# Optimization experiments

Hardware: AMD Instinct MI355X
Metric: run time of the kernel (lower is better)

Reference implementation:

```python
import jax, jax.numpy as jnp
import numpy as np

B, T, C = 4, 2048, 1024
H = 16
D = C // H  # head_dim = 64


def setup_inputs() -> dict:
    key = jax.random.key(0)
    ks = jax.random.split(key, 11)
    s = 0.02
    return {
        "q": jax.random.normal(ks[0], (B, T, C), jnp.float32),
        "k": jax.random.normal(ks[1], (B, T, C), jnp.float32),
        "v": jax.random.normal(ks[2], (B, T, C), jnp.float32),
        "Wq": jax.random.normal(ks[3], (C, C), jnp.float32) * s,
        "bq": jnp.zeros((C,), jnp.float32),
        "Wk": jax.random.normal(ks[4], (C, C), jnp.float32) * s,
        "bk": jnp.zeros((C,), jnp.float32),
        "Wv": jax.random.normal(ks[5], (C, C), jnp.float32) * s,
        "bv": jnp.zeros((C,), jnp.float32),
        "Wo": jax.random.normal(ks[6], (C, C), jnp.float32) * s,
        "bo": jnp.zeros((C,), jnp.float32),
    }


def reference(q, k, v, Wq, bq, Wk, bk, Wv, bv, Wo, bo):
    # projections (torch Linear: x @ W.T + b)
    qh = (q @ Wq.T + bq).reshape(B, T, H, D).transpose(0, 2, 1, 3)  # [B,H,T,D]
    kh = (k @ Wk.T + bk).reshape(B, T, H, D).transpose(0, 2, 1, 3)
    vh = (v @ Wv.T + bv).reshape(B, T, H, D).transpose(0, 2, 1, 3)
    scores = jnp.einsum('bhqd,bhkd->bhqk', qh, kh) * (D ** -0.5)  # [B,H,T,T]
    # causal mask (is_causal=True)
    causal = jnp.tril(jnp.ones((T, T), bool))
    scores = jnp.where(causal, scores, -jnp.inf)
    probs = jax.nn.softmax(scores, axis=-1)
    # dropout_rate=0.0 -> identity in eval mode
    out = jnp.einsum('bhqk,bhkd->bhqd', probs, vh)  # [B,H,T,D]
    out = out.transpose(0, 2, 1, 3).reshape(B, T, C)
    return out @ Wo.T + bo
```

## Files before the change

kernel.cpp:

```cpp
#include <hip/hip_runtime.h>
#include <hip/hip_bf16.h>

typedef __attribute__((ext_vector_type(8))) short bf16x8;
typedef __attribute__((ext_vector_type(4))) float f32x4;
typedef __attribute__((ext_vector_type(16))) float f32x16;

__device__ __forceinline__ unsigned short f2bf(float x) {
  union { float f; unsigned u; } v; v.f = x;
  unsigned r = v.u + 0x7fffu + ((v.u >> 16) & 1u);
  return (unsigned short)(r >> 16);
}

__device__ __forceinline__ unsigned cvtpk_bf16(float lo, float hi) {
  unsigned r;
  asm("v_cvt_pk_bf16_f32 %0, %1, %2" : "=v"(r) : "v"(lo), "v"(hi));
  return r;
}
__device__ __forceinline__ void pl32swap(unsigned &a, unsigned &b) {
  asm volatile("v_permlane32_swap_b32 %0, %1" : "+v"(a), "+v"(b));
}

__device__ __forceinline__ void gload_lds16(const void* g, void* l) {
  __builtin_amdgcn_global_load_lds((const __attribute__((address_space(1))) void*)g,
                                   (__attribute__((address_space(3))) void*)l, 16, 0, 0);
}

#define SWZ(x) ((x) ^ ((((x) >> 7) & 7) << 4))

__global__ __launch_bounds__(256) void cvt_w(
    const float* __restrict__ W0, const float* __restrict__ W1,
    const float* __restrict__ W2, const float* __restrict__ W3,
    unsigned short* __restrict__ o0, unsigned short* __restrict__ o1,
    unsigned short* __restrict__ o2, unsigned short* __restrict__ o3,
    float s0) {
  const int z = blockIdx.y;
  const float* W = (z == 0) ? W0 : (z == 1) ? W1 : (z == 2) ? W2 : W3;
  unsigned short* o = (z == 0) ? o0 : (z == 1) ? o1 : (z == 2) ? o2 : o3;
  const float s = (z == 0) ? s0 : 1.0f;
  const int i = blockIdx.x * 256 + threadIdx.x;
  const float4 x = ((const float4*)W)[i];
  uint2 u;
  u.x = cvtpk_bf16(x.x * s, x.y * s);
  u.y = cvtpk_bf16(x.z * s, x.w * s);
  ((uint2*)o)[i] = u;
}


__global__ __launch_bounds__(256) void proj_gemm3(
    const float* __restrict__ A0, const float* __restrict__ A1, const float* __restrict__ A2,
    const unsigned short* __restrict__ W0b, const unsigned short* __restrict__ W1b,
    const unsigned short* __restrict__ W2b,
    const float* __restrict__ b0, const float* __restrict__ b1, const float* __restrict__ b2,
    unsigned short* __restrict__ o0, unsigned short* __restrict__ o1,
    unsigned short* __restrict__ o2) {
  const int K = 1024;
  __shared__ __align__(16) unsigned short As[2][4096];
  __shared__ __align__(16) unsigned short Bs[2][4096];
  const int z = blockIdx.z;
  const float* A = (z == 0) ? A0 : (z == 1) ? A1 : A2;
  const unsigned short* Wb = (z == 0) ? W0b : (z == 1) ? W1b : W2b;
  const float* bias = (z == 0) ? b0 : (z == 1) ? b1 : b2;
  unsigned short* out = (z == 0) ? o0 : (z == 1) ? o1 : o2;
  const float bscale = (z == 0) ? 0.125f * 1.4426950408889634f : 1.0f;
  const int vtrans = (z == 2);

  const int tid = threadIdx.x;
  const int row0 = blockIdx.x * 128;
  const int col0 = blockIdx.y * 128;
  const int lane = tid & 63;
  const int w = tid >> 6;
  const int wm = (w >> 1) * 64, wn = (w & 1) * 64;
  const int fr = lane & 15;
  const int g = lane >> 4;
  const int frh = fr >> 1;
  const int gcf = ((fr & 1) * 4 + g) ^ frh;
  const int aoff = wm * 64 + frh * 128 + gcf * 16;
  const int boff = wn * 64 + frh * 128 + gcf * 16;

  const int ar = tid >> 2;
  const int acq = tid & 3;
  const float* asrc0 = &A[(size_t)(row0 + ar) * K + acq * 8];
  const float* asrc1 = asrc0 + (size_t)64 * K;
  const int awr = (ar >> 1) * 128 + ((((ar & 1) * 4 + acq) ^ ((ar >> 1) & 7)) * 16);

  const unsigned short* bsrc[2];
  int bldso[2];
#pragma unroll
  for (int j = 0; j < 2; ++j) {
    const int L = (w * 2 + j) * 64 + lane;
    const int pp = L >> 3, gc = L & 7;
    const int e = gc ^ (pp & 7);
    const int r = pp * 2 + (e >> 2), c = e & 3;
    bsrc[j] = Wb + (size_t)(col0 + r) * K + c * 8;
    bldso[j] = (w * 2 + j) * 1024;
  }

  f32x4 acc[4][4] = {};
  float4 la[4];

  auto loadA = [&](int kt) {
    const float* s0 = asrc0 + kt * 32;
    const float* s1 = asrc1 + kt * 32;
    la[0] = *(const float4*)s0; la[1] = *(const float4*)(s0 + 4);
    la[2] = *(const float4*)s1; la[3] = *(const float4*)(s1 + 4);
  };
  auto storeA = [&](int buf) {
    uint4 u0, u1;
    u0.x = cvtpk_bf16(la[0].x, la[0].y); u0.y = cvtpk_bf16(la[0].z, la[0].w);
    u0.z = cvtpk_bf16(la[1].x, la[1].y); u0.w = cvtpk_bf16(la[1].z, la[1].w);
    u1.x = cvtpk_bf16(la[2].x, la[2].y); u1.y = cvtpk_bf16(la[2].z, la[2].w);
    u1.z = cvtpk_bf16(la[3].x, la[3].y); u1.w = cvtpk_bf16(la[3].z, la[3].w);
    char* base = (char*)As[buf];
    *(uint4*)(base + awr) = u0;
    *(uint4*)(base + awr + 4096) = u1;
  };
  auto stageB = [&](int buf, int kt) {
#pragma unroll
    for (int j = 0; j < 2; ++j)
      gload_lds16(bsrc[j] + kt * 32, (char*)Bs[buf] + bldso[j]);
  };

  loadA(0); stageB(0, 0); storeA(0);
  __syncthreads();
  for (int kt = 0; kt < 32; ++kt) {
    const int buf = kt & 1;
    if (kt < 31) { loadA(kt + 1); stageB(buf ^ 1, kt + 1); }
    const char* Ab = (const char*)As[buf];
    const char* Bb = (const char*)Bs[buf];
    bf16x8 af[4], bfv[4];
#pragma unroll
    for (int i = 0; i < 4; ++i) {
      af[i] = *(const bf16x8*)(Ab + aoff + i * 1024);
      bfv[i] = *(const bf16x8*)(Bb + boff + i * 1024);
    }
#pragma unroll
    for (int i = 0; i < 4; ++i)
#pragma unroll
      for (int j = 0; j < 4; ++j)
        acc[i][j] = __builtin_amdgcn_mfma_f32_16x16x32_bf16(af[i], bfv[j], acc[i][j], 0, 0, 0);
    if (kt < 31) storeA(buf ^ 1);
    __syncthreads();
  }

#pragma unroll
  for (int j = 0; j < 4; ++j) {
    const int n = col0 + wn + j * 16 + fr;
    const float bv = bias[n] * bscale;
    const int h = n >> 6, d = n & 63;
#pragma unroll
    for (int i = 0; i < 4; ++i) {
      const int mrow = row0 + wm + i * 16 + g * 4;
      const int b = mrow >> 11, t0 = mrow & 2047;
      if (vtrans) {
        uint2 u;
        u.x = cvtpk_bf16(acc[i][j][0] + bv, acc[i][j][1] + bv);
        u.y = cvtpk_bf16(acc[i][j][2] + bv, acc[i][j][3] + bv);
        *(uint2*)(&out[(((size_t)b * 16 + h) * 64 + d) * 2048 + t0]) = u;
      } else {
#pragma unroll
        for (int r = 0; r < 4; ++r)
          out[(((size_t)b * 16 + h) * 2048 + (t0 + r)) * 64 + d] = f2bf(acc[i][j][r] + bv);
      }
    }
  }
}

__global__ __launch_bounds__(256) void out_gemm(
    const unsigned short* __restrict__ A, const unsigned short* __restrict__ Wb,
    const float* __restrict__ bias, float* __restrict__ out) {
  const int K = 1024;
  __shared__ __align__(16) unsigned short As[2][4096];
  __shared__ __align__(16) unsigned short Bs[2][4096];
  const int tid = threadIdx.x;
  const int row0 = blockIdx.x * 128;
  const int col0 = blockIdx.y * 128;
  const int lane = tid & 63;
  const int w = tid >> 6;
  const int wm = (w >> 1) * 64, wn = (w & 1) * 64;
  const int fr = lane & 15;
  const int g = lane >> 4;
  const int frh = fr >> 1;
  const int gcf = ((fr & 1) * 4 + g) ^ frh;
  const int aoff = wm * 64 + frh * 128 + gcf * 16;
  const int boff = wn * 64 + frh * 128 + gcf * 16;

  const unsigned short* asrc[2];
  const unsigned short* bsrc[2];
  int ldso[2];
#pragma unroll
  for (int j = 0; j < 2; ++j) {
    const int L = (w * 2 + j) * 64 + lane;
    const int pp = L >> 3, gc = L & 7;
    const int e = gc ^ (pp & 7);
    const int r = pp * 2 + (e >> 2), c = e & 3;
    asrc[j] = A + (size_t)(row0 + r) * K + c * 8;
    bsrc[j] = Wb + (size_t)(col0 + r) * K + c * 8;
    ldso[j] = (w * 2 + j) * 1024;
  }

  f32x4 acc[4][4] = {};

  auto stage = [&](int buf, int kt) {
#pragma unroll
    for (int j = 0; j < 2; ++j) {
      gload_lds16(asrc[j] + kt * 32, (char*)As[buf] + ldso[j]);
      gload_lds16(bsrc[j] + kt * 32, (char*)Bs[buf] + ldso[j]);
    }
  };

  stage(0, 0);
  __syncthreads();
  for (int kt = 0; kt < 32; ++kt) {
    const int buf = kt & 1;
    if (kt < 31) stage(buf ^ 1, kt + 1);
    const char* Ab = (const char*)As[buf];
    const char* Bb = (const char*)Bs[buf];
    bf16x8 af[4], bfv[4];
#pragma unroll
    for (int i = 0; i < 4; ++i) {
      af[i] = *(const bf16x8*)(Ab + aoff + i * 1024);
      bfv[i] = *(const bf16x8*)(Bb + boff + i * 1024);
    }
#pragma unroll
    for (int i = 0; i < 4; ++i)
#pragma unroll
      for (int j = 0; j < 4; ++j)
        acc[i][j] = __builtin_amdgcn_mfma_f32_16x16x32_bf16(af[i], bfv[j], acc[i][j], 0, 0, 0);
    __syncthreads();
  }

#pragma unroll
  for (int j = 0; j < 4; ++j) {
    const int n = col0 + wn + j * 16 + fr;
    const float bv = bias[n];
#pragma unroll
    for (int i = 0; i < 4; ++i) {
      const int mrow = row0 + wm + i * 16 + g * 4;
#pragma unroll
      for (int r = 0; r < 4; ++r)
        out[(size_t)(mrow + r) * 1024 + n] = acc[i][j][r] + bv;
    }
  }
}

__global__ __launch_bounds__(256) void attn_mfma(
    const unsigned short* __restrict__ qh, const unsigned short* __restrict__ kh,
    const unsigned short* __restrict__ vT, unsigned short* __restrict__ Ob) {
  __shared__ __align__(16) unsigned short Klds[2][64 * 64];
  __shared__ __align__(16) unsigned short Vlds[2][64 * 64];

  const int tid = threadIdx.x;
  const int lane = tid & 63;
  const int w = tid >> 6;
  const int bh = blockIdx.y;
  const int b = bh >> 4, h = bh & 15;
  const int q32 = lane & 31;
  const int hi = lane >> 5;

  const char* kbase = (const char*)(kh + (size_t)bh * 2048 * 64);
  const char* vbase = (const char*)(vT + (size_t)bh * 64 * 2048);

  const int lrow = lane >> 3;
  const int cb = (((lane & 7) ^ lrow) << 4);

  auto stage = [&](int buf, int t) {
    const int kv0 = t * 64;
#pragma unroll
    for (int j = 0; j < 2; ++j) {
      const int c = w * 2 + j;
      const int r = c * 8 + lrow;
      gload_lds16(kbase + (size_t)(kv0 + r) * 128 + cb,
                  (char*)Klds[buf] + c * 1024);
      gload_lds16(vbase + (size_t)r * 4096 + (size_t)kv0 * 2 + cb,
                  (char*)Vlds[buf] + c * 1024);
    }
  };

  for (int pass = 0; pass < 2; ++pass) {
    const int qt = pass == 0 ? (15 - (int)blockIdx.x) : (int)blockIdx.x;
    const int qb = qt * 128 + w * 32;
    const int nt = 2 * qt + 2;

    bf16x8 qf[4];
    {
      const unsigned short* qp = qh + ((size_t)bh * 2048 + qb + q32) * 64;
#pragma unroll
      for (int kk = 0; kk < 4; ++kk)
        qf[kk] = *(const bf16x8*)(qp + kk * 16 + hi * 8);
    }

    f32x16 acc_o[2] = {};
    float m_run = -INFINITY, l_run = 0.f;

    stage(0, 0);
    __syncthreads();

    int cur = 0;
    for (int t = 0; t < nt; ++t) {
      const int kv0 = t * 64;
      if (t + 1 < nt) stage(cur ^ 1, t + 1);

      if (kv0 < qb + 32) {
        const char* Kb = (const char*)Klds[cur];
        const char* Vb = (const char*)Vlds[cur];

        f32x16 sacc[2] = {};
        __builtin_amdgcn_s_setprio(1);
#pragma unroll
        for (int kk = 0; kk < 4; ++kk) {
          bf16x8 kf0 = *(const bf16x8*)(Kb + SWZ((q32) * 128 + kk * 32 + hi * 16));
          bf16x8 kf1 = *(const bf16x8*)(Kb + SWZ((32 + q32) * 128 + kk * 32 + hi * 16));
          sacc[0] = __builtin_amdgcn_mfma_f32_32x32x16_bf16(kf0, qf[kk], sacc[0], 0, 0, 0);
          sacc[1] = __builtin_amdgcn_mfma_f32_32x32x16_bf16(kf1, qf[kk], sacc[1], 0, 0, 0);
        }
        __builtin_amdgcn_s_setprio(0);

        if (kv0 + 64 > qb) {
          const int qa = qb + q32;
#pragma unroll
          for (int mkv = 0; mkv < 2; ++mkv)
#pragma unroll
            for (int r = 0; r < 16; ++r) {
              const int kva = kv0 + mkv * 32 + 4 * hi + (r & 3) + 8 * (r >> 2);
              if (kva > qa) sacc[mkv][r] = -INFINITY;
            }
        }

        float mx = -INFINITY;
#pragma unroll
        for (int mkv = 0; mkv < 2; ++mkv)
#pragma unroll
          for (int r = 0; r < 16; ++r) mx = fmaxf(mx, sacc[mkv][r]);
        mx = fmaxf(mx, __shfl_xor(mx, 32));
        if (!__all(mx <= m_run + 8.f)) {
          const float mnew = fmaxf(m_run, mx);
          const float al = exp2f(m_run - mnew);
          m_run = mnew;
          l_run *= al;
          acc_o[0] = acc_o[0] * al;
          acc_o[1] = acc_o[1] * al;
        }

        float ls = 0.f;
        unsigned W[2][8];
#pragma unroll
        for (int mkv = 0; mkv < 2; ++mkv)
#pragma unroll
          for (int s = 0; s < 8; ++s) {
            const float p0 = exp2f(sacc[mkv][2 * s] - m_run);
            const float p1 = exp2f(sacc[mkv][2 * s + 1] - m_run);
            ls += p0 + p1;
            W[mkv][s] = cvtpk_bf16(p0, p1);
          }
        ls += __shfl_xor(ls, 32);
        l_run += ls;

#pragma unroll
        for (int mkv = 0; mkv < 2; ++mkv) {
          pl32swap(W[mkv][0], W[mkv][2]);
          pl32swap(W[mkv][1], W[mkv][3]);
          pl32swap(W[mkv][4], W[mkv][6]);
          pl32swap(W[mkv][5], W[mkv][7]);
        }

        __builtin_amdgcn_s_setprio(1);
#pragma unroll
        for (int wg = 0; wg < 4; ++wg) {
          union { unsigned u[4]; bf16x8 v; } pk;
          pk.u[0] = W[wg >> 1][(wg & 1) * 4 + 0];
          pk.u[1] = W[wg >> 1][(wg & 1) * 4 + 1];
          pk.u[2] = W[wg >> 1][(wg & 1) * 4 + 2];
          pk.u[3] = W[wg >> 1][(wg & 1) * 4 + 3];
          bf16x8 vf0 = *(const bf16x8*)(Vb + SWZ((q32) * 128 + wg * 32 + hi * 16));
          bf16x8 vf1 = *(const bf16x8*)(Vb + SWZ((32 + q32) * 128 + wg * 32 + hi * 16));
          acc_o[0] = __builtin_amdgcn_mfma_f32_32x32x16_bf16(vf0, pk.v, acc_o[0], 0, 0, 0);
          acc_o[1] = __builtin_amdgcn_mfma_f32_32x32x16_bf16(vf1, pk.v, acc_o[1], 0, 0, 0);
        }
        __builtin_amdgcn_s_setprio(0);
      }

      __syncthreads();
      cur ^= 1;
    }

    {
      const float inv = 1.0f / l_run;
      const int qa = qb + q32;
      unsigned short* op = Ob + ((size_t)b * 2048 + qa) * 1024 + h * 64;
#pragma unroll
      for (int md = 0; md < 2; ++md)
#pragma unroll
        for (int rr = 0; rr < 4; ++rr) {
          uint2 u;
          u.x = cvtpk_bf16(acc_o[md][rr * 4 + 0] * inv, acc_o[md][rr * 4 + 1] * inv);
          u.y = cvtpk_bf16(acc_o[md][rr * 4 + 2] * inv, acc_o[md][rr * 4 + 3] * inv);
          *(uint2*)(op + md * 32 + rr * 8 + hi * 4) = u;
        }
    }
  }
}

extern "C" void kernel_launch(void* const* d_in, const int* in_sizes, int n_in,
                              void* d_out, int out_size, void* d_ws, size_t ws_size,
                              hipStream_t stream) {
  (void)in_sizes; (void)n_in; (void)out_size; (void)ws_size;
  const float* q = (const float*)d_in[0];
  const float* k = (const float*)d_in[1];
  const float* v = (const float*)d_in[2];
  const float* Wq = (const float*)d_in[3];
  const float* bq = (const float*)d_in[4];
  const float* Wk = (const float*)d_in[5];
  const float* bk = (const float*)d_in[6];
  const float* Wv = (const float*)d_in[7];
  const float* bv = (const float*)d_in[8];
  const float* Wo = (const float*)d_in[9];
  const float* bo = (const float*)d_in[10];
  float* out = (float*)d_out;

  const size_t SZ = (size_t)4 * 16 * 2048 * 64;
  const size_t WSZ = (size_t)1024 * 1024;
  unsigned short* qh = (unsigned short*)d_ws;
  unsigned short* kh = qh + SZ;
  unsigned short* vT = kh + SZ;
  unsigned short* Ob = vT + SZ;
  unsigned short* Wqb = Ob + SZ;
  unsigned short* Wkb = Wqb + WSZ;
  unsigned short* Wvb = Wkb + WSZ;
  unsigned short* Wob = Wvb + WSZ;

  dim3 g0(1024, 4), b0(256);
  cvt_w<<<g0, b0, 0, stream>>>(Wq, Wk, Wv, Wo, Wqb, Wkb, Wvb, Wob,
                               0.125f * 1.4426950408889634f);

  dim3 g1(64, 8, 3), b1(256);
  proj_gemm3<<<g1, b1, 0, stream>>>(q, k, v, Wqb, Wkb, Wvb, bq, bk, bv, qh, kh, vT);

  dim3 g2(8, 64), b2(256);
  attn_mfma<<<g2, b2, 0, stream>>>(qh, kh, vT, Ob);

  dim3 g3(64, 8), b3(256);
  out_gemm<<<g3, b3, 0, stream>>>(Ob, Wob, bo, out);
}
```

Measured before the change: 223.7 us.

## Triple-buffer LDS in projection and output GEMMs with explicit vmcnt waits

Both projection and output GEMMs move from double to triple LDS buffering. Each now prefetches two k-tiles ahead and uses manual s_waitcnt vmcnt plus raw s_barrier instead of __syncthreads. The projection GEMM ping-pongs two register sets for the fp32 A loads so conversion and storing lag one tile behind the loads. This aims to hide global load latency behind MFMA work, at the cost of more LDS per block, which may lower occupancy, and fragile hand-counted wait values.

```diff
diff --git a/kernel.cpp b/kernel.cpp
--- a/kernel.cpp
+++ b/kernel.cpp
@@ -19,7 +19,6 @@
 __device__ __forceinline__ void pl32swap(unsigned &a, unsigned &b) {
   asm volatile("v_permlane32_swap_b32 %0, %1" : "+v"(a), "+v"(b));
 }
-
 __device__ __forceinline__ void gload_lds16(const void* g, void* l) {
   __builtin_amdgcn_global_load_lds((const __attribute__((address_space(1))) void*)g,
                                    (__attribute__((address_space(3))) void*)l, 16, 0, 0);
@@ -54,8 +53,9 @@
     unsigned short* __restrict__ o0, unsigned short* __restrict__ o1,
     unsigned short* __restrict__ o2) {
   const int K = 1024;
-  __shared__ __align__(16) unsigned short As[2][4096];
-  __shared__ __align__(16) unsigned short Bs[2][4096];
+  const int NK = 32;
+  __shared__ __align__(16) unsigned short As[3][4096];
+  __shared__ __align__(16) unsigned short Bs[3][4096];
   const int z = blockIdx.z;
   const float* A = (z == 0) ? A0 : (z == 1) ? A1 : A2;
   const unsigned short* Wb = (z == 0) ? W0b : (z == 1) ? W1b : W2b;
@@ -96,51 +96,92 @@
   }
 
   f32x4 acc[4][4] = {};
-  float4 la[4];
-
-  auto loadA = [&](int kt) {
-    const float* s0 = asrc0 + kt * 32;
-    const float* s1 = asrc1 + kt * 32;
-    la[0] = *(const float4*)s0; la[1] = *(const float4*)(s0 + 4);
-    la[2] = *(const float4*)s1; la[3] = *(const float4*)(s1 + 4);
-  };
-  auto storeA = [&](int buf) {
-    uint4 u0, u1;
-    u0.x = cvtpk_bf16(la[0].x, la[0].y); u0.y = cvtpk_bf16(la[0].z, la[0].w);
-    u0.z = cvtpk_bf16(la[1].x, la[1].y); u0.w = cvtpk_bf16(la[1].z, la[1].w);
-    u1.x = cvtpk_bf16(la[2].x, la[2].y); u1.y = cvtpk_bf16(la[2].z, la[2].w);
-    u1.z = cvtpk_bf16(la[3].x, la[3].y); u1.w = cvtpk_bf16(la[3].z, la[3].w);
-    char* base = (char*)As[buf];
-    *(uint4*)(base + awr) = u0;
-    *(uint4*)(base + awr + 4096) = u1;
-  };
-  auto stageB = [&](int buf, int kt) {
-#pragma unroll
-    for (int j = 0; j < 2; ++j)
-      gload_lds16(bsrc[j] + kt * 32, (char*)Bs[buf] + bldso[j]);
-  };
-
-  loadA(0); stageB(0, 0); storeA(0);
-  __syncthreads();
-  for (int kt = 0; kt < 32; ++kt) {
-    const int buf = kt & 1;
-    if (kt < 31) { loadA(kt + 1); stageB(buf ^ 1, kt + 1); }
-    const char* Ab = (const char*)As[buf];
-    const char* Bb = (const char*)Bs[buf];
-    bf16x8 af[4], bfv[4];
-#pragma unroll
-    for (int i = 0; i < 4; ++i) {
-      af[i] = *(const bf16x8*)(Ab + aoff + i * 1024);
-      bfv[i] = *(const bf16x8*)(Bb + boff + i * 1024);
-    }
-#pragma unroll
-    for (int i = 0; i < 4; ++i)
-#pragma unroll
-      for (int j = 0; j < 4; ++j)
-        acc[i][j] = __builtin_amdgcn_mfma_f32_16x16x32_bf16(af[i], bfv[j], acc[i][j], 0, 0, 0);
-    if (kt < 31) storeA(buf ^ 1);
-    __syncthreads();
-  }
+  float4 la0[4], la1[4];
+
+#define LOADA(kt, LA)                                        \
+  {                                                          \
+    const float* s0_ = asrc0 + (kt) * 32;                    \
+    const float* s1_ = asrc1 + (kt) * 32;                    \
+    LA[0] = *(const float4*)s0_; LA[1] = *(const float4*)(s0_ + 4); \
+    LA[2] = *(const float4*)s1_; LA[3] = *(const float4*)(s1_ + 4); \
+  }
+#define STOREA(buf, LA)                                               \
+  {                                                                   \
+    uint4 u0_, u1_;                                                   \
+    u0_.x = cvtpk_bf16(LA[0].x, LA[0].y); u0_.y = cvtpk_bf16(LA[0].z, LA[0].w); \
+    u0_.z = cvtpk_bf16(LA[1].x, LA[1].y); u0_.w = cvtpk_bf16(LA[1].z, LA[1].w); \
+    u1_.x = cvtpk_bf16(LA[2].x, LA[2].y); u1_.y = cvtpk_bf16(LA[2].z, LA[2].w); \
+    u1_.z = cvtpk_bf16(LA[3].x, LA[3].y); u1_.w = cvtpk_bf16(LA[3].z, LA[3].w); \
+    char* base_ = (char*)As[buf];                                     \
+    *(uint4*)(base_ + awr) = u0_;                                     \
+    *(uint4*)(base_ + awr + 4096) = u1_;                              \
+  }
+#define STAGEB(buf, kt)                                               \
+  {                                                                   \
+    gload_lds16(bsrc[0] + (kt) * 32, (char*)Bs[buf] + bldso[0]);      \
+    gload_lds16(bsrc[1] + (kt) * 32, (char*)Bs[buf] + bldso[1]);      \
+  }
+#define COMPUTE(cb)                                                   \
+  {                                                                   \
+    const char* Ab_ = (const char*)As[cb];                            \
+    const char* Bb_ = (const char*)Bs[cb];                            \
+    bf16x8 af[4], bfv[4];                                             \
+    _Pragma("unroll")                                                 \
+    for (int i = 0; i < 4; ++i) {                                     \
+      af[i] = *(const bf16x8*)(Ab_ + aoff + i * 1024);                \
+      bfv[i] = *(const bf16x8*)(Bb_ + boff + i * 1024);               \
+    }                                                                 \
+    _Pragma("unroll")                                                 \
+    for (int i = 0; i < 4; ++i)                                       \
+      _Pragma("unroll")                                               \
+      for (int j = 0; j < 4; ++j)                                     \
+        acc[i][j] = __builtin_amdgcn_mfma_f32_16x16x32_bf16(af[i], bfv[j], acc[i][j], 0, 0, 0); \
+  }
+
+  STAGEB(0, 0); STAGEB(1, 1);
+  LOADA(0, la0); LOADA(1, la1);
+  STOREA(0, la0);
+  asm volatile("s_waitcnt lgkmcnt(0)" ::: "memory");
+
+  int cur = 0;
+  for (int kt = 0; kt < NK; kt += 2) {
+    if (kt == 0) asm volatile("s_waitcnt vmcnt(0)" ::: "memory");
+    else         asm volatile("s_waitcnt vmcnt(6)" ::: "memory");
+    __builtin_amdgcn_sched_barrier(0);
+    __builtin_amdgcn_s_barrier();
+    __builtin_amdgcn_sched_barrier(0);
+    {
+      const int nx1 = (cur == 2) ? 0 : cur + 1;
+      const int nx2 = (nx1 == 2) ? 0 : nx1 + 1;
+      if (kt + 2 < NK) { LOADA(kt + 2, la0); STAGEB(nx2, kt + 2); }
+      __builtin_amdgcn_sched_barrier(0);
+      COMPUTE(cur);
+      STOREA(nx1, la1);
+      asm volatile("s_waitcnt lgkmcnt(0)" ::: "memory");
+      cur = nx1;
+    }
+    if (kt + 1 == NK - 1) asm volatile("s_waitcnt vmcnt(0)" ::: "memory");
+    else                  asm volatile("s_waitcnt vmcnt(6)" ::: "memory");
+    __builtin_amdgcn_sched_barrier(0);
+    __builtin_amdgcn_s_barrier();
+    __builtin_amdgcn_sched_barrier(0);
+    {
+      const int nx1 = (cur == 2) ? 0 : cur + 1;
+      const int nx2 = (nx1 == 2) ? 0 : nx1 + 1;
+      if (kt + 3 < NK) { LOADA(kt + 3, la1); STAGEB(nx2, kt + 3); }
+      __builtin_amdgcn_sched_barrier(0);
+      COMPUTE(cur);
+      if (kt + 2 < NK) {
+        STOREA(nx1, la0);
+        asm volatile("s_waitcnt lgkmcnt(0)" ::: "memory");
+      }
+      cur = nx1;
+    }
+  }
+#undef LOADA
+#undef STOREA
+#undef STAGEB
+#undef COMPUTE
 
 #pragma unroll
   for (int j = 0; j < 4; ++j) {
@@ -169,8 +210,9 @@
     const unsigned short* __restrict__ A, const unsigned short* __restrict__ Wb,
     const float* __restrict__ bias, float* __restrict__ out) {
   const int K = 1024;
-  __shared__ __align__(16) unsigned short As[2][4096];
-  __shared__ __align__(16) unsigned short Bs[2][4096];
+  const int NK = 32;
+  __shared__ __align__(16) unsigned short As[3][4096];
+  __shared__ __align__(16) unsigned short Bs[3][4096];
   const int tid = threadIdx.x;
   const int row0 = blockIdx.x * 128;
   const int col0 = blockIdx.y * 128;
@@ -208,13 +250,20 @@
     }
   };
 
-  stage(0, 0);
-  __syncthreads();
-  for (int kt = 0; kt < 32; ++kt) {
-    const int buf = kt & 1;
-    if (kt < 31) stage(buf ^ 1, kt + 1);
-    const char* Ab = (const char*)As[buf];
-    const char* Bb = (const char*)Bs[buf];
+  stage(0, 0); stage(1, 1);
+  int cur = 0;
+  for (int kt = 0; kt < NK; ++kt) {
+    if (kt == 0 || kt == NK - 1) asm volatile("s_waitcnt vmcnt(0)" ::: "memory");
+    else                         asm volatile("s_waitcnt vmcnt(4)" ::: "memory");
+    __builtin_amdgcn_sched_barrier(0);
+    __builtin_amdgcn_s_barrier();
+    __builtin_amdgcn_sched_barrier(0);
+    const int nx1 = (cur == 2) ? 0 : cur + 1;
+    const int nx2 = (nx1 == 2) ? 0 : nx1 + 1;
+    if (kt + 2 < NK) stage(nx2, kt + 2);
+    __builtin_amdgcn_sched_barrier(0);
+    const char* Ab = (const char*)As[cur];
+    const char* Bb = (const char*)Bs[cur];
     bf16x8 af[4], bfv[4];
 #pragma unroll
     for (int i = 0; i < 4; ++i) {
@@ -226,7 +275,7 @@
 #pragma unroll
       for (int j = 0; j < 4; ++j)
         acc[i][j] = __builtin_amdgcn_mfma_f32_16x16x32_bf16(af[i], bfv[j], acc[i][j], 0, 0, 0);
-    __syncthreads();
+    cur = nx1;
   }
 
 #pragma unroll
```

Result: faster. 201.2 us (-10.1%).

## Pre-convert activations to bf16 and use direct-to-LDS loads with BK=64 tiles

Applied to the files above, without the earlier changes.

Adds a separate kernel that converts the q/k/v fp32 activations to bf16 in workspace. The projection GEMM can then stage A through global_load_lds like B, instead of loading fp32 into registers, converting, and storing to LDS. Both GEMMs double the K-tile to 64, halving the number of barriers, and raise wave priority around the MFMA blocks. The cost is an extra launch plus a full fp32 read and bf16 write/read of the activations, and twice the LDS per block.

```diff
diff --git a/kernel.cpp b/kernel.cpp
--- a/kernel.cpp
+++ b/kernel.cpp
@@ -19,7 +19,6 @@
 __device__ __forceinline__ void pl32swap(unsigned &a, unsigned &b) {
   asm volatile("v_permlane32_swap_b32 %0, %1" : "+v"(a), "+v"(b));
 }
-
 __device__ __forceinline__ void gload_lds16(const void* g, void* l) {
   __builtin_amdgcn_global_load_lds((const __attribute__((address_space(1))) void*)g,
                                    (__attribute__((address_space(3))) void*)l, 16, 0, 0);
@@ -45,19 +44,37 @@
   ((uint2*)o)[i] = u;
 }
 
+__global__ __launch_bounds__(256) void cvt_x(
+    const float* __restrict__ q, const float* __restrict__ k,
+    const float* __restrict__ v,
+    unsigned short* __restrict__ oq, unsigned short* __restrict__ ok,
+    unsigned short* __restrict__ ov) {
+  const int z = blockIdx.y;
+  const float* X = (z == 0) ? q : (z == 1) ? k : v;
+  unsigned short* o = (z == 0) ? oq : (z == 1) ? ok : ov;
+  const int i = blockIdx.x * 256 + threadIdx.x;
+  const float4 x = ((const float4*)X)[i];
+  uint2 u;
+  u.x = cvtpk_bf16(x.x, x.y);
+  u.y = cvtpk_bf16(x.z, x.w);
+  ((uint2*)o)[i] = u;
+}
+
 
 __global__ __launch_bounds__(256) void proj_gemm3(
-    const float* __restrict__ A0, const float* __restrict__ A1, const float* __restrict__ A2,
+    const unsigned short* __restrict__ X0, const unsigned short* __restrict__ X1,
+    const unsigned short* __restrict__ X2,
     const unsigned short* __restrict__ W0b, const unsigned short* __restrict__ W1b,
     const unsigned short* __restrict__ W2b,
     const float* __restrict__ b0, const float* __restrict__ b1, const float* __restrict__ b2,
     unsigned short* __restrict__ o0, unsigned short* __restrict__ o1,
     unsigned short* __restrict__ o2) {
   const int K = 1024;
-  __shared__ __align__(16) unsigned short As[2][4096];
-  __shared__ __align__(16) unsigned short Bs[2][4096];
+  const int NK = 16;
+  __shared__ __align__(16) unsigned short As[2][8192];
+  __shared__ __align__(16) unsigned short Bs[2][8192];
   const int z = blockIdx.z;
-  const float* A = (z == 0) ? A0 : (z == 1) ? A1 : A2;
+  const unsigned short* A = (z == 0) ? X0 : (z == 1) ? X1 : X2;
   const unsigned short* Wb = (z == 0) ? W0b : (z == 1) ? W1b : W2b;
   const float* bias = (z == 0) ? b0 : (z == 1) ? b1 : b2;
   unsigned short* out = (z == 0) ? o0 : (z == 1) ? o1 : o2;
@@ -77,68 +94,55 @@
   const int aoff = wm * 64 + frh * 128 + gcf * 16;
   const int boff = wn * 64 + frh * 128 + gcf * 16;
 
-  const int ar = tid >> 2;
-  const int acq = tid & 3;
-  const float* asrc0 = &A[(size_t)(row0 + ar) * K + acq * 8];
-  const float* asrc1 = asrc0 + (size_t)64 * K;
-  const int awr = (ar >> 1) * 128 + ((((ar & 1) * 4 + acq) ^ ((ar >> 1) & 7)) * 16);
-
+  const unsigned short* asrc[2];
   const unsigned short* bsrc[2];
-  int bldso[2];
+  int ldo[2];
 #pragma unroll
   for (int j = 0; j < 2; ++j) {
     const int L = (w * 2 + j) * 64 + lane;
     const int pp = L >> 3, gc = L & 7;
     const int e = gc ^ (pp & 7);
     const int r = pp * 2 + (e >> 2), c = e & 3;
+    asrc[j] = A + (size_t)(row0 + r) * K + c * 8;
     bsrc[j] = Wb + (size_t)(col0 + r) * K + c * 8;
-    bldso[j] = (w * 2 + j) * 1024;
+    ldo[j] = (w * 2 + j) * 1024;
   }
 
   f32x4 acc[4][4] = {};
-  float4 la[4];
-
-  auto loadA = [&](int kt) {
-    const float* s0 = asrc0 + kt * 32;
-    const float* s1 = asrc1 + kt * 32;
-    la[0] = *(const float4*)s0; la[1] = *(const float4*)(s0 + 4);
-    la[2] = *(const float4*)s1; la[3] = *(const float4*)(s1 + 4);
+
+  auto stage = [&](int buf, int kt) {
+#pragma unroll
+    for (int h = 0; h < 2; ++h)
+#pragma unroll
+      for (int j = 0; j < 2; ++j) {
+        gload_lds16(asrc[j] + kt * 64 + h * 32, (char*)As[buf] + h * 8192 + ldo[j]);
+        gload_lds16(bsrc[j] + kt * 64 + h * 32, (char*)Bs[buf] + h * 8192 + ldo[j]);
+      }
   };
-  auto storeA = [&](int buf) {
-    uint4 u0, u1;
-    u0.x = cvtpk_bf16(la[0].x, la[0].y); u0.y = cvtpk_bf16(la[0].z, la[0].w);
-    u0.z = cvtpk_bf16(la[1].x, la[1].y); u0.w = cvtpk_bf16(la[1].z, la[1].w);
-    u1.x = cvtpk_bf16(la[2].x, la[2].y); u1.y = cvtpk_bf16(la[2].z, la[2].w);
-    u1.z = cvtpk_bf16(la[3].x, la[3].y); u1.w = cvtpk_bf16(la[3].z, la[3].w);
-    char* base = (char*)As[buf];
-    *(uint4*)(base + awr) = u0;
-    *(uint4*)(base + awr + 4096) = u1;
-  };
-  auto stageB = [&](int buf, int kt) {
-#pragma unroll
-    for (int j = 0; j < 2; ++j)
-      gload_lds16(bsrc[j] + kt * 32, (char*)Bs[buf] + bldso[j]);
-  };
-
-  loadA(0); stageB(0, 0); storeA(0);
+
+  stage(0, 0);
   __syncthreads();
-  for (int kt = 0; kt < 32; ++kt) {
+  for (int kt = 0; kt < NK; ++kt) {
     const int buf = kt & 1;
-    if (kt < 31) { loadA(kt + 1); stageB(buf ^ 1, kt + 1); }
-    const char* Ab = (const char*)As[buf];
-    const char* Bb = (const char*)Bs[buf];
-    bf16x8 af[4], bfv[4];
-#pragma unroll
-    for (int i = 0; i < 4; ++i) {
-      af[i] = *(const bf16x8*)(Ab + aoff + i * 1024);
-      bfv[i] = *(const bf16x8*)(Bb + boff + i * 1024);
-    }
-#pragma unroll
-    for (int i = 0; i < 4; ++i)
-#pragma unroll
-      for (int j = 0; j < 4; ++j)
-        acc[i][j] = __builtin_amdgcn_mfma_f32_16x16x32_bf16(af[i], bfv[j], acc[i][j], 0, 0, 0);
-    if (kt < 31) storeA(buf ^ 1);
+    if (kt + 1 < NK) stage(buf ^ 1, kt + 1);
+#pragma unroll
+    for (int h = 0; h < 2; ++h) {
+      const char* Ab = (const char*)As[buf] + h * 8192;
+      const char* Bb = (const char*)Bs[buf] + h * 8192;
+      bf16x8 af[4], bfv[4];
+#pragma unroll
+      for (int i = 0; i < 4; ++i) {
+        af[i] = *(const bf16x8*)(Ab + aoff + i * 1024);
+        bfv[i] = *(const bf16x8*)(Bb + boff + i * 1024);
+      }
+      __builtin_amdgcn_s_setprio(1);
+#pragma unroll
+      for (int i = 0; i < 4; ++i)
+#pragma unroll
+        for (int j = 0; j < 4; ++j)
+          acc[i][j] = __builtin_amdgcn_mfma_f32_16x16x32_bf16(af[i], bfv[j], acc[i][j], 0, 0, 0);
+      __builtin_amdgcn_s_setprio(0);
+    }
     __syncthreads();
   }
 
@@ -169,8 +173,9 @@
     const unsigned short* __restrict__ A, const unsigned short* __restrict__ Wb,
     const float* __restrict__ bias, float* __restrict__ out) {
   const int K = 1024;
-  __shared__ __align__(16) unsigned short As[2][4096];
-  __shared__ __align__(16) unsigned short Bs[2][4096];
+  const int NK = 16;
+  __shared__ __align__(16) unsigned short As[2][8192];
+  __shared__ __align__(16) unsigned short Bs[2][8192];
   const int tid = threadIdx.x;
   const int row0 = blockIdx.x * 128;
   const int col0 = blockIdx.y * 128;
@@ -186,7 +191,7 @@
 
   const unsigned short* asrc[2];
   const unsigned short* bsrc[2];
-  int ldso[2];
+  int ldo[2];
 #pragma unroll
   for (int j = 0; j < 2; ++j) {
     const int L = (w * 2 + j) * 64 + lane;
@@ -195,37 +200,44 @@
     const int r = pp * 2 + (e >> 2), c = e & 3;
     asrc[j] = A + (size_t)(row0 + r) * K + c * 8;
     bsrc[j] = Wb + (size_t)(col0 + r) * K + c * 8;
-    ldso[j] = (w * 2 + j) * 1024;
+    ldo[j] = (w * 2 + j) * 1024;
   }
 
   f32x4 acc[4][4] = {};
 
   auto stage = [&](int buf, int kt) {
 #pragma unroll
-    for (int j = 0; j < 2; ++j) {
-      gload_lds16(asrc[j] + kt * 32, (char*)As[buf] + ldso[j]);
-      gload_lds16(bsrc[j] + kt * 32, (char*)Bs[buf] + ldso[j]);
-    }
+    for (int h = 0; h < 2; ++h)
+#pragma unroll
+      for (int j = 0; j < 2; ++j) {
+        gload_lds16(asrc[j] + kt * 64 + h * 32, (char*)As[buf] + h * 8192 + ldo[j]);
+        gload_lds16(bsrc[j] + kt * 64 + h * 32, (char*)Bs[buf] + h * 8192 + ldo[j]);
+      }
   };
 
   stage(0, 0);
   __syncthreads();
-  for (int kt = 0; kt < 32; ++kt) {
+  for (int kt = 0; kt < NK; ++kt) {
     const int buf = kt & 1;
-    if (kt < 31) stage(buf ^ 1, kt + 1);
-    const char* Ab = (const char*)As[buf];
-    const char* Bb = (const char*)Bs[buf];
-    bf16x8 af[4], bfv[4];
-#pragma unroll
-    for (int i = 0; i < 4; ++i) {
-      af[i] = *(const bf16x8*)(Ab + aoff + i * 1024);
-      bfv[i] = *(const bf16x8*)(Bb + boff + i * 1024);
-    }
-#pragma unroll
-    for (int i = 0; i < 4; ++i)
-#pragma unroll
-      for (int j = 0; j < 4; ++j)
-        acc[i][j] = __builtin_amdgcn_mfma_f32_16x16x32_bf16(af[i], bfv[j], acc[i][j], 0, 0, 0);
+    if (kt + 1 < NK) stage(buf ^ 1, kt + 1);
+#pragma unroll
+    for (int h = 0; h < 2; ++h) {
+      const char* Ab = (const char*)As[buf] + h * 8192;
+      const char* Bb = (const char*)Bs[buf] + h * 8192;
+      bf16x8 af[4], bfv[4];
+#pragma unroll
+      for (int i = 0; i < 4; ++i) {
+        af[i] = *(const bf16x8*)(Ab + aoff + i * 1024);
+        bfv[i] = *(const bf16x8*)(Bb + boff + i * 1024);
+      }
+      __builtin_amdgcn_s_setprio(1);
+#pragma unroll
+      for (int i = 0; i < 4; ++i)
+#pragma unroll
+        for (int j = 0; j < 4; ++j)
+          acc[i][j] = __builtin_amdgcn_mfma_f32_16x16x32_bf16(af[i], bfv[j], acc[i][j], 0, 0, 0);
+      __builtin_amdgcn_s_setprio(0);
+    }
     __syncthreads();
   }
 
@@ -419,21 +431,27 @@
 
   const size_t SZ = (size_t)4 * 16 * 2048 * 64;
   const size_t WSZ = (size_t)1024 * 1024;
-  unsigned short* qh = (unsigned short*)d_ws;
+  unsigned short* qx = (unsigned short*)d_ws;
+  unsigned short* kx = qx + SZ;
+  unsigned short* vx = kx + SZ;
+  unsigned short* qh = vx + SZ;
   unsigned short* kh = qh + SZ;
   unsigned short* vT = kh + SZ;
-  unsigned short* Ob = vT + SZ;
-  unsigned short* Wqb = Ob + SZ;
+  unsigned short* Wqb = vT + SZ;
   unsigned short* Wkb = Wqb + WSZ;
   unsigned short* Wvb = Wkb + WSZ;
   unsigned short* Wob = Wvb + WSZ;
+  unsigned short* Ob = qx;
 
   dim3 g0(1024, 4), b0(256);
   cvt_w<<<g0, b0, 0, stream>>>(Wq, Wk, Wv, Wo, Wqb, Wkb, Wvb, Wob,
                                0.125f * 1.4426950408889634f);
+  dim3 gx(8192, 3), bx(256);
+  cvt_x<<<gx, bx, 0, stream>>>(q, k, v, qx, kx, vx);
 
   dim3 g1(64, 8, 3), b1(256);
-  proj_gemm3<<<g1, b1, 0, stream>>>(q, k, v, Wqb, Wkb, Wvb, bq, bk, bv, qh, kh, vT);
+  proj_gemm3<<<g1, b1, 0, stream>>>(qx, kx, vx, Wqb, Wkb, Wvb, bq, bk, bv,
+                                    qh, kh, vT);
 
   dim3 g2(8, 64), b2(256);
   attn_mfma<<<g2, b2, 0, stream>>>(qh, kh, vT, Ob);
```

Result: faster. 210.9 us (-5.7%).
